# Kernel optimization log

Measured on AMD Instinct MI355X. Metric: run time of the kernel, lower is better.

Reference implementation:

```python
import jax, jax.numpy as jnp
import numpy as np

NUM_HEADS = 16
THETA = 10000.0


def _rope(x, pos):
    # x: [B, H, S, d_k], pos: [S] int. Rotate consecutive pairs (even, odd).
    d = x.shape[-1]
    inv_freq = THETA ** (-jnp.arange(0, d, 2, dtype=jnp.float32) / d)  # [d/2]
    ang = pos.astype(jnp.float32)[:, None] * inv_freq                  # [S, d/2]
    cos, sin = jnp.cos(ang), jnp.sin(ang)
    x1, x2 = x[..., 0::2], x[..., 1::2]
    out = jnp.stack([x1 * cos - x2 * sin, x1 * sin + x2 * cos], axis=-1)
    return out.reshape(x.shape)


def setup_inputs() -> dict:
    key = jax.random.key(0)
    k1, k2, k3 = jax.random.split(key, 3)
    B, S, D = 2, 2048, 1024
    x = jax.random.normal(k1, (B, S, D), dtype=jnp.float32)
    # scale weights like a trained init so attention logits are well-behaved
    W_qkv = jax.random.normal(k2, (3 * D, D), dtype=jnp.float32) * 0.02
    W_out = jax.random.normal(k3, (D, D), dtype=jnp.float32) * 0.02
    return {"x": x, "W_qkv": W_qkv, "W_out": W_out}


def reference(x, W_qkv, W_out):
    B, S, D = x.shape
    H = NUM_HEADS
    dk = D // H

    qkv = x @ W_qkv.T                                   # [B, S, 3D]
    q, k, v = jnp.split(qkv, 3, axis=-1)

    def to_heads(t):
        return t.reshape(B, S, H, dk).transpose(0, 2, 1, 3)  # [B, H, S, dk]

    q, k, v = to_heads(q), to_heads(k), to_heads(v)

    pos = jnp.arange(S)
    q = _rope(q, pos)
    k = _rope(k, pos)

    scale = 1.0 / jnp.sqrt(jnp.asarray(dk, dtype=x.dtype))
    logits = jnp.einsum('bhqd,bhkd->bhqk', q, k) * scale  # [B, H, S, S]
    causal = jnp.tril(jnp.ones((S, S), dtype=bool))
    logits = jnp.where(causal, logits, -jnp.inf)
    attn = jax.nn.softmax(logits, axis=-1)
    heads = jnp.einsum('bhqk,bhkd->bhqd', attn, v)        # [B, H, S, dk]
    merged = heads.transpose(0, 2, 1, 3).reshape(B, S, D)
    return merged @ W_out.T
```

## Files before the change

### kernel.cpp

```cpp
#include <hip/hip_runtime.h>
#include <hip/hip_bf16.h>
#include <math.h>

#define BATCH   2
#define SEQ     2048
#define DMODEL  1024
#define NHEAD   16
#define DK      64
#define MTOK    (BATCH*SEQ)
#define QKVN    (3*DMODEL)
#define BH      (BATCH*NHEAD)

typedef __attribute__((ext_vector_type(8)))  __bf16 bf16x8;
typedef __attribute__((ext_vector_type(4)))  float  f32x4;
typedef __attribute__((ext_vector_type(16))) float  f32x16;

#define GL16(gp, lp) __builtin_amdgcn_global_load_lds( \
    (const __attribute__((address_space(1))) unsigned int*)(gp), \
    (__attribute__((address_space(3))) unsigned int*)(lp), 16, 0, 0)

__global__ __launch_bounds__(256) void cvt_bf16(const float* __restrict__ in,
                                                __hip_bfloat16* __restrict__ out, int n) {
    int i = (blockIdx.x * 256 + threadIdx.x) * 4;
    if (i >= n) return;
    float4 v = *(const float4*)(in + i);
    __hip_bfloat162 a, b;
    a.x = __float2bfloat16(v.x); a.y = __float2bfloat16(v.y);
    b.x = __float2bfloat16(v.z); b.y = __float2bfloat16(v.w);
    *(__hip_bfloat162*)(out + i)     = a;
    *(__hip_bfloat162*)(out + i + 2) = b;
}

#define GBM 128
#define GBN 128
#define GBK 32

template<int OUT_BF16>
__global__ __launch_bounds__(256) void gemm_bf16_nt(const __hip_bfloat16* __restrict__ A,
                                                    const __hip_bfloat16* __restrict__ B,
                                                    void* __restrict__ Cv,
                                                    int M, int N, int K) {
    __shared__ __align__(16) __hip_bfloat16 As[GBM][GBK];
    __shared__ __align__(16) __hip_bfloat16 Bs[GBN][GBK];
    const int tid  = threadIdx.x;
    const int wid  = tid >> 6;
    const int lane = tid & 63;
    const int fr   = lane & 15;
    const int fq   = lane >> 4;
    const int wm   = (wid >> 1) * 64;
    const int wn   = (wid & 1) * 64;
    const int m0   = blockIdx.y * GBM;
    const int n0   = blockIdx.x * GBN;

    f32x4 acc[4][4];
#pragma unroll
    for (int m = 0; m < 4; m++)
#pragma unroll
        for (int n = 0; n < 4; n++) acc[m][n] = (f32x4)0.f;

    const __hip_bfloat16* a0 = A + (size_t)(m0 + (tid >> 2)) * K + (tid & 3) * 8;
    const __hip_bfloat16* a1 = a0 + (size_t)64 * K;
    const __hip_bfloat16* b0 = B + (size_t)(n0 + (tid >> 2)) * K + (tid & 3) * 8;
    const __hip_bfloat16* b1 = b0 + (size_t)64 * K;
    __hip_bfloat16* asd0 = &As[0][0] + tid * 8;
    __hip_bfloat16* asd1 = asd0 + 2048;
    __hip_bfloat16* bsd0 = &Bs[0][0] + tid * 8;
    __hip_bfloat16* bsd1 = bsd0 + 2048;

    const __hip_bfloat16* ArP = &As[wm + fr][0] + fq * 8;
    const __hip_bfloat16* BrP = &Bs[wn + fr][0] + fq * 8;

    for (int k0 = 0; k0 < K; k0 += GBK) {
        GL16(a0 + k0, asd0);
        GL16(a1 + k0, asd1);
        GL16(b0 + k0, bsd0);
        GL16(b1 + k0, bsd1);
        __syncthreads();

        bf16x8 af[4], bfv[4];
#pragma unroll
        for (int m = 0; m < 4; m++) af[m]  = *(const bf16x8*)(ArP + m * 512);
#pragma unroll
        for (int n = 0; n < 4; n++) bfv[n] = *(const bf16x8*)(BrP + n * 512);
#pragma unroll
        for (int m = 0; m < 4; m++)
#pragma unroll
            for (int n = 0; n < 4; n++)
                acc[m][n] = __builtin_amdgcn_mfma_f32_16x16x32_bf16(af[m], bfv[n], acc[m][n], 0, 0, 0);
        __syncthreads();
    }

#pragma unroll
    for (int m = 0; m < 4; m++)
#pragma unroll
        for (int n = 0; n < 4; n++)
#pragma unroll
            for (int r = 0; r < 4; r++) {
                size_t row = m0 + wm + m * 16 + fq * 4 + r;
                size_t col = n0 + wn + n * 16 + fr;
                if (OUT_BF16)
                    ((__hip_bfloat16*)Cv)[row * N + col] = __float2bfloat16(acc[m][n][r]);
                else
                    ((float*)Cv)[row * N + col] = acc[m][n][r];
            }
}

__global__ __launch_bounds__(256) void rope_qk(const __hip_bfloat16* __restrict__ qkvb,
                                               __hip_bfloat16* __restrict__ qh,
                                               __hip_bfloat16* __restrict__ kh) {
    int idx  = blockIdx.x * 256 + threadIdx.x;
    int row  = idx >> 10;
    int p    = idx & 1023;
    int half = p >> 9;
    int pp   = p & 511;
    int hh   = pp >> 5;
    int j    = pp & 31;
    int b    = row >> 11, s = row & (SEQ - 1);
    const __hip_bfloat16* src = qkvb + (size_t)row * QKVN + half * DMODEL + hh * DK + 2 * j;
    __hip_bfloat162 xv = *(const __hip_bfloat162*)src;
    float x1 = __bfloat162float(xv.x);
    float x2 = __bfloat162float(xv.y);
    float inv = exp2f(-(float)j * 0.41524101186092030f);
    float ang = (float)s * inv;
    float sn, cs;
    sincosf(ang, &sn, &cs);
    float sc = half ? 1.0f : 0.125f;
    __hip_bfloat162 o;
    o.x = __float2bfloat16((x1 * cs - x2 * sn) * sc);
    o.y = __float2bfloat16((x1 * sn + x2 * cs) * sc);
    __hip_bfloat16* dst = (half ? kh : qh) + ((size_t)(b * NHEAD + hh) * SEQ + s) * DK + 2 * j;
    *(__hip_bfloat162*)dst = o;
}

__global__ __launch_bounds__(256) void v_trans(const __hip_bfloat16* __restrict__ qkvb,
                                               __hip_bfloat16* __restrict__ vt) {
    __shared__ __hip_bfloat16 Ts[64][72];
    const int t  = threadIdx.x;
    const int s0 = blockIdx.x * 64;
    const int bh = blockIdx.y;
    const int b  = bh >> 4, h = bh & 15;
    const int sl = t >> 3;
    const int dc = (t & 7) * 8;
#pragma unroll
    for (int i = 0; i < 2; i++) {
        int s = sl + i * 32;
        bf16x8 v = *(const bf16x8*)&qkvb[(size_t)(b * SEQ + s0 + s) * QKVN + 2 * DMODEL + h * DK + dc];
        *(bf16x8*)&Ts[s][dc] = v;
    }
    __syncthreads();
    const int dl = t >> 3;
    const int sc = (t & 7) * 8;
#pragma unroll
    for (int i = 0; i < 2; i++) {
        int d = dl + i * 32;
        bf16x8 o;
#pragma unroll
        for (int j = 0; j < 8; j++) o[j] = *(const __bf16*)&Ts[sc + j][d];
        *(bf16x8*)&vt[(size_t)bh * DK * SEQ + (size_t)d * SEQ + s0 + sc] = o;
    }
}

static __device__ inline unsigned pack_bf16(float lo, float hi) {
    __hip_bfloat162 t;
    t.x = __float2bfloat16(lo);
    t.y = __float2bfloat16(hi);
    return *reinterpret_cast<unsigned*>(&t);
}

__global__ __launch_bounds__(128) void attn_mfma(const __hip_bfloat16* __restrict__ qh,
                                                 const __hip_bfloat16* __restrict__ kh,
                                                 const __hip_bfloat16* __restrict__ vt,
                                                 __hip_bfloat16* __restrict__ mergedb) {
    __shared__ __align__(16) __hip_bfloat16 Ob[2][32][72];
    const int tid  = threadIdx.x;
    const int wid  = tid >> 6;
    const int lane = tid & 63;
    const int qr   = lane & 31;
    const int hi   = lane >> 5;
    const int bid  = blockIdx.x;
    const int j    = bid >> 5;
    const int bh   = bid & 31;
    const int b    = bh >> 4, h = bh & 15;

    const int w    = wid ? (63 - j) : j;
    const int q0   = w * 32;
    const int nsub = w + 1;

    const __hip_bfloat16* Qb = qh + (size_t)bh * SEQ * DK;
    const __hip_bfloat16* Kb = kh + (size_t)bh * SEQ * DK;
    const __hip_bfloat16* Vb = vt + (size_t)bh * DK * SEQ;

    bf16x8 qf[4];
#pragma unroll
    for (int i = 0; i < 4; i++)
        qf[i] = *(const bf16x8*)&Qb[(size_t)(q0 + qr) * DK + 16 * i + 8 * hi];

    f32x16 acc0 = (f32x16)0.f, acc1 = (f32x16)0.f;
    float m = -1e30f, lsum = 0.f;

    bf16x8 kf[4];
#pragma unroll
    for (int i = 0; i < 4; i++)
        kf[i] = *(const bf16x8*)&Kb[(size_t)qr * DK + 16 * i + 8 * hi];

    union PW { unsigned w[4]; bf16x8 v; };

    for (int s = 0; s < nsub; s++) {
        const int keybase = s * 32;
        f32x16 st = (f32x16)0.f;
        __builtin_amdgcn_s_setprio(1);
#pragma unroll
        for (int i = 0; i < 4; i++)
            st = __builtin_amdgcn_mfma_f32_32x32x16_bf16(kf[i], qf[i], st, 0, 0, 0);
        __builtin_amdgcn_s_setprio(0);

        if (s + 1 < nsub) {
#pragma unroll
            for (int i = 0; i < 4; i++)
                kf[i] = *(const bf16x8*)&Kb[(size_t)(keybase + 32 + qr) * DK + 16 * i + 8 * hi];
        }
        bf16x8 va[2][2];
#pragma unroll
        for (int dt = 0; dt < 2; dt++)
#pragma unroll
            for (int t = 0; t < 2; t++)
                va[dt][t] = *(const bf16x8*)&Vb[(size_t)(dt * 32 + qr) * SEQ + keybase + t * 16 + hi * 8];

        if (s == nsub - 1) {
#pragma unroll
            for (int r = 0; r < 16; r++) {
                int kl = (r & 3) + 8 * (r >> 2) + 4 * hi;
                if (kl > qr) st[r] = -INFINITY;
            }
        }

        float mx = st[0];
#pragma unroll
        for (int r = 1; r < 16; r++) mx = fmaxf(mx, st[r]);
        mx = fmaxf(mx, __shfl_xor(mx, 32));
        float mnew = fmaxf(m, mx);
        float corr = __expf(m - mnew);
        m = mnew;
        float ps = 0.f;
#pragma unroll
        for (int r = 0; r < 16; r++) {
            float pv = __expf(st[r] - mnew);
            st[r] = pv;
            ps += pv;
        }
        ps += __shfl_xor(ps, 32);
        lsum = lsum * corr + ps;
#pragma unroll
        for (int r = 0; r < 16; r++) { acc0[r] *= corr; acc1[r] *= corr; }

        unsigned c[8];
#pragma unroll
        for (int k2 = 0; k2 < 8; k2++)
            c[k2] = pack_bf16(st[2 * k2], st[2 * k2 + 1]);
        unsigned p0 = __shfl_xor(c[0], 32);
        unsigned p1 = __shfl_xor(c[1], 32);
        unsigned p2 = __shfl_xor(c[2], 32);
        unsigned p3 = __shfl_xor(c[3], 32);
        unsigned p4 = __shfl_xor(c[4], 32);
        unsigned p5 = __shfl_xor(c[5], 32);
        unsigned p6 = __shfl_xor(c[6], 32);
        unsigned p7 = __shfl_xor(c[7], 32);
        PW pa[2];
        pa[0].w[0] = hi ? p2 : c[0];
        pa[0].w[1] = hi ? p3 : c[1];
        pa[0].w[2] = hi ? c[2] : p0;
        pa[0].w[3] = hi ? c[3] : p1;
        pa[1].w[0] = hi ? p6 : c[4];
        pa[1].w[1] = hi ? p7 : c[5];
        pa[1].w[2] = hi ? c[6] : p4;
        pa[1].w[3] = hi ? c[7] : p5;

        __builtin_amdgcn_s_setprio(1);
#pragma unroll
        for (int t = 0; t < 2; t++) {
            acc0 = __builtin_amdgcn_mfma_f32_32x32x16_bf16(va[0][t], pa[t].v, acc0, 0, 0, 0);
            acc1 = __builtin_amdgcn_mfma_f32_32x32x16_bf16(va[1][t], pa[t].v, acc1, 0, 0, 0);
        }
        __builtin_amdgcn_s_setprio(0);
    }

    float invl = 1.0f / lsum;
#pragma unroll
    for (int r = 0; r < 16; r += 2) {
        int d = (r & 3) + 8 * (r >> 2) + 4 * hi;
        *(unsigned*)&Ob[wid][qr][d]      = pack_bf16(acc0[r] * invl, acc0[r + 1] * invl);
        *(unsigned*)&Ob[wid][qr][d + 32] = pack_bf16(acc1[r] * invl, acc1[r + 1] * invl);
    }
    __builtin_amdgcn_wave_barrier();
#pragma unroll
    for (int p = 0; p < 4; p++) {
        int row = p * 8 + (lane >> 3);
        int col = (lane & 7) * 8;
        bf16x8 ov = *(const bf16x8*)&Ob[wid][row][col];
        *(bf16x8*)&mergedb[(size_t)(b * SEQ + q0 + row) * DMODEL + h * DK + col] = ov;
    }
}

extern "C" void kernel_launch(void* const* d_in, const int* in_sizes, int n_in,
                              void* d_out, int out_size, void* d_ws, size_t ws_size,
                              hipStream_t stream) {
    const float* x    = (const float*)d_in[0];
    const float* Wqkv = (const float*)d_in[1];
    const float* Wout = (const float*)d_in[2];
    float* out = (float*)d_out;

    char* w = (char*)d_ws;
    __hip_bfloat16* qkvb   = (__hip_bfloat16*)(w);
    __hip_bfloat16* qh     = (__hip_bfloat16*)(w + (24u << 20));
    __hip_bfloat16* kh     = (__hip_bfloat16*)(w + (32u << 20));
    __hip_bfloat16* vt     = (__hip_bfloat16*)(w + (40u << 20));
    __hip_bfloat16* xb     = (__hip_bfloat16*)(w + (48u << 20));
    __hip_bfloat16* merged = (__hip_bfloat16*)(w + (48u << 20));
    __hip_bfloat16* wqkvb  = (__hip_bfloat16*)(w + (56u << 20));
    __hip_bfloat16* woutb  = (__hip_bfloat16*)(w + (62u << 20));

    cvt_bf16<<<MTOK * DMODEL / 1024, 256, 0, stream>>>(x, xb, MTOK * DMODEL);
    cvt_bf16<<<QKVN * DMODEL / 1024, 256, 0, stream>>>(Wqkv, wqkvb, QKVN * DMODEL);
    cvt_bf16<<<DMODEL * DMODEL / 1024, 256, 0, stream>>>(Wout, woutb, DMODEL * DMODEL);

    dim3 g1(QKVN / GBN, MTOK / GBM);
    gemm_bf16_nt<1><<<g1, 256, 0, stream>>>(xb, wqkvb, qkvb, MTOK, QKVN, DMODEL);

    rope_qk<<<MTOK * 1024 / 256, 256, 0, stream>>>(qkvb, qh, kh);
    v_trans<<<dim3(SEQ / 64, BH), 256, 0, stream>>>(qkvb, vt);

    attn_mfma<<<1024, 128, 0, stream>>>(qh, kh, vt, merged);

    dim3 g3(DMODEL / GBN, MTOK / GBM);
    gemm_bf16_nt<0><<<g3, 256, 0, stream>>>(merged, woutb, out, MTOK, DMODEL, DMODEL);
}
```

Baseline: 233.3 us.

## Software-pipeline QK MFMA with softmax, use exp2 and lazy rescale in attention

Folds log2(e) into the Q scaling so softmax can use exp2f directly. The rescale of the running max is skipped unless the new max exceeds the old one by a threshold, and the per-iteration row-sum shuffle is deferred to a single reduction at the end. The key loop is software-pipelined so the next tile's QK MFMAs run while the current tile's softmax and PV are computed, with the causal tile peeled out of the loop. Blocks shrink to one wave each, launched longest-first. This trades per-block load balancing via paired waves for more blocks and a larger live register set.

```diff
diff --git a/kernel.cpp b/kernel.cpp
--- a/kernel.cpp
+++ b/kernel.cpp
@@ -124,7 +124,7 @@
     float ang = (float)s * inv;
     float sn, cs;
     sincosf(ang, &sn, &cs);
-    float sc = half ? 1.0f : 0.125f;
+    float sc = half ? 1.0f : 0.18033688011112042f;
     __hip_bfloat162 o;
     o.x = __float2bfloat16((x1 * cs - x2 * sn) * sc);
     o.y = __float2bfloat16((x1 * sn + x2 * cs) * sc);
@@ -167,22 +167,19 @@
     return *reinterpret_cast<unsigned*>(&t);
 }
 
-__global__ __launch_bounds__(128) void attn_mfma(const __hip_bfloat16* __restrict__ qh,
-                                                 const __hip_bfloat16* __restrict__ kh,
-                                                 const __hip_bfloat16* __restrict__ vt,
-                                                 __hip_bfloat16* __restrict__ mergedb) {
-    __shared__ __align__(16) __hip_bfloat16 Ob[2][32][72];
-    const int tid  = threadIdx.x;
-    const int wid  = tid >> 6;
-    const int lane = tid & 63;
+__global__ __launch_bounds__(64) void attn_mfma(const __hip_bfloat16* __restrict__ qh,
+                                                const __hip_bfloat16* __restrict__ kh,
+                                                const __hip_bfloat16* __restrict__ vt,
+                                                __hip_bfloat16* __restrict__ mergedb) {
+    __shared__ __align__(16) __hip_bfloat16 Ob[32][72];
+    const int lane = threadIdx.x;
     const int qr   = lane & 31;
     const int hi   = lane >> 5;
     const int bid  = blockIdx.x;
-    const int j    = bid >> 5;
     const int bh   = bid & 31;
     const int b    = bh >> 4, h = bh & 15;
 
-    const int w    = wid ? (63 - j) : j;
+    const int w    = 63 - (bid >> 5);
     const int q0   = w * 32;
     const int nsub = w + 1;
 
@@ -198,27 +195,80 @@
     f32x16 acc0 = (f32x16)0.f, acc1 = (f32x16)0.f;
     float m = -1e30f, lsum = 0.f;
 
+    union PW { unsigned w[4]; bf16x8 v; };
+
+#define SOFTMAX(ST)                                                            \
+    {                                                                          \
+        float mx = ST[0];                                                      \
+        _Pragma("unroll")                                                      \
+        for (int r = 1; r < 16; r++) mx = fmaxf(mx, ST[r]);                    \
+        mx = fmaxf(mx, __shfl_xor(mx, 32));                                    \
+        if (!__all(mx <= m + 11.5415603f)) {                                   \
+            float mnew = fmaxf(m, mx);                                         \
+            float corr = exp2f(m - mnew);                                      \
+            m = mnew;                                                          \
+            lsum *= corr;                                                      \
+            _Pragma("unroll")                                                  \
+            for (int r = 0; r < 16; r++) { acc0[r] *= corr; acc1[r] *= corr; } \
+        }                                                                      \
+        float ps = 0.f;                                                        \
+        _Pragma("unroll")                                                      \
+        for (int r = 0; r < 16; r++) {                                         \
+            float pv = exp2f(ST[r] - m);                                       \
+            ST[r] = pv;                                                        \
+            ps += pv;                                                          \
+        }                                                                      \
+        lsum += ps;                                                            \
+    }
+
+#define PACK_PV(ST, VA)                                                        \
+    {                                                                          \
+        unsigned c0 = pack_bf16(ST[0],  ST[1]);                                \
+        unsigned c1 = pack_bf16(ST[2],  ST[3]);                                \
+        unsigned c2 = pack_bf16(ST[4],  ST[5]);                                \
+        unsigned c3 = pack_bf16(ST[6],  ST[7]);                                \
+        unsigned c4 = pack_bf16(ST[8],  ST[9]);                                \
+        unsigned c5 = pack_bf16(ST[10], ST[11]);                               \
+        unsigned c6 = pack_bf16(ST[12], ST[13]);                               \
+        unsigned c7 = pack_bf16(ST[14], ST[15]);                               \
+        unsigned e0 = __shfl_xor(hi ? c0 : c2, 32);                            \
+        unsigned e1 = __shfl_xor(hi ? c1 : c3, 32);                            \
+        unsigned e2 = __shfl_xor(hi ? c4 : c6, 32);                            \
+        unsigned e3 = __shfl_xor(hi ? c5 : c7, 32);                            \
+        PW pa0, pa1;                                                           \
+        pa0.w[0] = hi ? e0 : c0;                                               \
+        pa0.w[1] = hi ? e1 : c1;                                               \
+        pa0.w[2] = hi ? c2 : e0;                                               \
+        pa0.w[3] = hi ? c3 : e1;                                               \
+        pa1.w[0] = hi ? e2 : c4;                                               \
+        pa1.w[1] = hi ? e3 : c5;                                               \
+        pa1.w[2] = hi ? c6 : e2;                                               \
+        pa1.w[3] = hi ? c7 : e3;                                               \
+        __builtin_amdgcn_s_setprio(1);                                         \
+        acc0 = __builtin_amdgcn_mfma_f32_32x32x16_bf16(VA[0][0], pa0.v, acc0, 0, 0, 0); \
+        acc1 = __builtin_amdgcn_mfma_f32_32x32x16_bf16(VA[1][0], pa0.v, acc1, 0, 0, 0); \
+        acc0 = __builtin_amdgcn_mfma_f32_32x32x16_bf16(VA[0][1], pa1.v, acc0, 0, 0, 0); \
+        acc1 = __builtin_amdgcn_mfma_f32_32x32x16_bf16(VA[1][1], pa1.v, acc1, 0, 0, 0); \
+        __builtin_amdgcn_s_setprio(0);                                         \
+    }
+
     bf16x8 kf[4];
 #pragma unroll
     for (int i = 0; i < 4; i++)
         kf[i] = *(const bf16x8*)&Kb[(size_t)qr * DK + 16 * i + 8 * hi];
-
-    union PW { unsigned w[4]; bf16x8 v; };
-
-    for (int s = 0; s < nsub; s++) {
+    f32x16 st = (f32x16)0.f;
+    __builtin_amdgcn_s_setprio(1);
+#pragma unroll
+    for (int i = 0; i < 4; i++)
+        st = __builtin_amdgcn_mfma_f32_32x32x16_bf16(kf[i], qf[i], st, 0, 0, 0);
+    __builtin_amdgcn_s_setprio(0);
+
+    for (int s = 0; s < nsub - 1; s++) {
         const int keybase = s * 32;
-        f32x16 st = (f32x16)0.f;
-        __builtin_amdgcn_s_setprio(1);
+        bf16x8 kf2[4];
 #pragma unroll
         for (int i = 0; i < 4; i++)
-            st = __builtin_amdgcn_mfma_f32_32x32x16_bf16(kf[i], qf[i], st, 0, 0, 0);
-        __builtin_amdgcn_s_setprio(0);
-
-        if (s + 1 < nsub) {
-#pragma unroll
-            for (int i = 0; i < 4; i++)
-                kf[i] = *(const bf16x8*)&Kb[(size_t)(keybase + 32 + qr) * DK + 16 * i + 8 * hi];
-        }
+            kf2[i] = *(const bf16x8*)&Kb[(size_t)(keybase + 32 + qr) * DK + 16 * i + 8 * hi];
         bf16x8 va[2][2];
 #pragma unroll
         for (int dt = 0; dt < 2; dt++)
@@ -226,79 +276,54 @@
             for (int t = 0; t < 2; t++)
                 va[dt][t] = *(const bf16x8*)&Vb[(size_t)(dt * 32 + qr) * SEQ + keybase + t * 16 + hi * 8];
 
-        if (s == nsub - 1) {
-#pragma unroll
-            for (int r = 0; r < 16; r++) {
-                int kl = (r & 3) + 8 * (r >> 2) + 4 * hi;
-                if (kl > qr) st[r] = -INFINITY;
-            }
+        SOFTMAX(st);
+
+        f32x16 st2 = (f32x16)0.f;
+        __builtin_amdgcn_s_setprio(1);
+#pragma unroll
+        for (int i = 0; i < 4; i++)
+            st2 = __builtin_amdgcn_mfma_f32_32x32x16_bf16(kf2[i], qf[i], st2, 0, 0, 0);
+        __builtin_amdgcn_s_setprio(0);
+
+        PACK_PV(st, va);
+        st = st2;
+    }
+
+    {
+        const int keybase = (nsub - 1) * 32;
+        bf16x8 va[2][2];
+#pragma unroll
+        for (int dt = 0; dt < 2; dt++)
+#pragma unroll
+            for (int t = 0; t < 2; t++)
+                va[dt][t] = *(const bf16x8*)&Vb[(size_t)(dt * 32 + qr) * SEQ + keybase + t * 16 + hi * 8];
+#pragma unroll
+        for (int r = 0; r < 16; r++) {
+            int kl = (r & 3) + 8 * (r >> 2) + 4 * hi;
+            if (kl > qr) st[r] = -INFINITY;
         }
-
-        float mx = st[0];
-#pragma unroll
-        for (int r = 1; r < 16; r++) mx = fmaxf(mx, st[r]);
-        mx = fmaxf(mx, __shfl_xor(mx, 32));
-        float mnew = fmaxf(m, mx);
-        float corr = __expf(m - mnew);
-        m = mnew;
-        float ps = 0.f;
-#pragma unroll
-        for (int r = 0; r < 16; r++) {
-            float pv = __expf(st[r] - mnew);
-            st[r] = pv;
-            ps += pv;
-        }
-        ps += __shfl_xor(ps, 32);
-        lsum = lsum * corr + ps;
-#pragma unroll
-        for (int r = 0; r < 16; r++) { acc0[r] *= corr; acc1[r] *= corr; }
-
-        unsigned c[8];
-#pragma unroll
-        for (int k2 = 0; k2 < 8; k2++)
-            c[k2] = pack_bf16(st[2 * k2], st[2 * k2 + 1]);
-        unsigned p0 = __shfl_xor(c[0], 32);
-        unsigned p1 = __shfl_xor(c[1], 32);
-        unsigned p2 = __shfl_xor(c[2], 32);
-        unsigned p3 = __shfl_xor(c[3], 32);
-        unsigned p4 = __shfl_xor(c[4], 32);
-        unsigned p5 = __shfl_xor(c[5], 32);
-        unsigned p6 = __shfl_xor(c[6], 32);
-        unsigned p7 = __shfl_xor(c[7], 32);
-        PW pa[2];
-        pa[0].w[0] = hi ? p2 : c[0];
-        pa[0].w[1] = hi ? p3 : c[1];
-        pa[0].w[2] = hi ? c[2] : p0;
-        pa[0].w[3] = hi ? c[3] : p1;
-        pa[1].w[0] = hi ? p6 : c[4];
-        pa[1].w[1] = hi ? p7 : c[5];
-        pa[1].w[2] = hi ? c[6] : p4;
-        pa[1].w[3] = hi ? c[7] : p5;
-
-        __builtin_amdgcn_s_setprio(1);
-#pragma unroll
-        for (int t = 0; t < 2; t++) {
-            acc0 = __builtin_amdgcn_mfma_f32_32x32x16_bf16(va[0][t], pa[t].v, acc0, 0, 0, 0);
-            acc1 = __builtin_amdgcn_mfma_f32_32x32x16_bf16(va[1][t], pa[t].v, acc1, 0, 0, 0);
-        }
-        __builtin_amdgcn_s_setprio(0);
-    }
-
+        SOFTMAX(st);
+        PACK_PV(st, va);
+    }
+
+    lsum += __shfl_xor(lsum, 32);
     float invl = 1.0f / lsum;
 #pragma unroll
     for (int r = 0; r < 16; r += 2) {
         int d = (r & 3) + 8 * (r >> 2) + 4 * hi;
-        *(unsigned*)&Ob[wid][qr][d]      = pack_bf16(acc0[r] * invl, acc0[r + 1] * invl);
-        *(unsigned*)&Ob[wid][qr][d + 32] = pack_bf16(acc1[r] * invl, acc1[r + 1] * invl);
+        *(unsigned*)&Ob[qr][d]      = pack_bf16(acc0[r] * invl, acc0[r + 1] * invl);
+        *(unsigned*)&Ob[qr][d + 32] = pack_bf16(acc1[r] * invl, acc1[r + 1] * invl);
     }
     __builtin_amdgcn_wave_barrier();
 #pragma unroll
     for (int p = 0; p < 4; p++) {
         int row = p * 8 + (lane >> 3);
         int col = (lane & 7) * 8;
-        bf16x8 ov = *(const bf16x8*)&Ob[wid][row][col];
+        bf16x8 ov = *(const bf16x8*)&Ob[row][col];
         *(bf16x8*)&mergedb[(size_t)(b * SEQ + q0 + row) * DMODEL + h * DK + col] = ov;
     }
+#undef SOFTMAX
+#undef PACK_PV
 }
 
 extern "C" void kernel_launch(void* const* d_in, const int* in_sizes, int n_in,
@@ -329,7 +354,7 @@
     rope_qk<<<MTOK * 1024 / 256, 256, 0, stream>>>(qkvb, qh, kh);
     v_trans<<<dim3(SEQ / 64, BH), 256, 0, stream>>>(qkvb, vt);
 
-    attn_mfma<<<1024, 128, 0, stream>>>(qh, kh, vt, merged);
+    attn_mfma<<<2048, 64, 0, stream>>>(qh, kh, vt, merged);
 
     dim3 g3(DMODEL / GBN, MTOK / GBM);
     gemm_bf16_nt<0><<<g3, 256, 0, stream>>>(merged, woutb, out, MTOK, DMODEL, DMODEL);
```

New measurement: 231.8 us. No clear change (-0.6%).
